# Kernel tuning notes

Measured on AMD Instinct MI355X. Metric: run time of the kernel, lower is better.

## Reference

```python
import jax, jax.numpy as jnp
import numpy as np
from jax import lax

T, B, F, H, C = 1024, 128, 88, 1024, 88


def setup_inputs() -> dict:
    key = jax.random.key(0)
    ks = jax.random.split(key, 8)
    s = 0.02
    lengths = jnp.sort(jax.random.randint(ks[1], (B,), 1, T + 1))[::-1]  # descending, as pack_padded requires
    return {
        "input_sequences": jax.random.normal(ks[0], (T, B, F), dtype=jnp.float32),
        "input_sequence_lengths": lengths.astype(jnp.int64),
        "W_ih": jax.random.normal(ks[2], (4 * H, F), dtype=jnp.float32) * s,
        "W_hh": jax.random.normal(ks[3], (4 * H, H), dtype=jnp.float32) * s,
        "b_ih": jax.random.normal(ks[4], (4 * H,), dtype=jnp.float32) * s,
        "b_hh": jax.random.normal(ks[5], (4 * H,), dtype=jnp.float32) * s,
        "W_fc": jax.random.normal(ks[6], (C, H), dtype=jnp.float32) * s,
        "b_fc": jax.random.normal(ks[7], (C,), dtype=jnp.float32) * s,
    }


def reference(input_sequences, input_sequence_lengths, W_ih, W_hh, b_ih, b_hh, W_fc, b_fc):
    Tn, Bn, _ = input_sequences.shape
    Hn = W_hh.shape[1]
    # mask[t, b] = True iff timestep t is within sequence b (equivalent to :batch_size_t slicing
    # when lengths are sorted descending, as the torch code assumes)
    mask_seq = jnp.arange(Tn)[:, None] < input_sequence_lengths[None, :]  # [T, B]

    h0 = jnp.zeros((Bn, Hn), dtype=input_sequences.dtype)
    c0 = jnp.zeros((Bn, Hn), dtype=input_sequences.dtype)

    def step(carry, inp):
        h, c = carry
        x, m = inp  # x: [B, F], m: [B]
        gates = x @ W_ih.T + b_ih + h @ W_hh.T + b_hh  # [B, 4H], order i,f,g,o
        i, f, g, o = jnp.split(gates, 4, axis=1)
        c_new = jax.nn.sigmoid(f) * c + jax.nn.sigmoid(i) * jnp.tanh(g)
        h_new = jax.nn.sigmoid(o) * jnp.tanh(c_new)
        mb = m[:, None]
        h2 = jnp.where(mb, h_new, h)
        c2 = jnp.where(mb, c_new, c)
        logits_t = jnp.where(mb, h2 @ W_fc.T + b_fc, 0.0)  # rows beyond batch_size_t stay zero
        return (h2, c2), logits_t

    (_, _), predictions = lax.scan(step, (h0, c0), (input_sequences, mask_seq))  # [T, B, C]

    logits = jnp.transpose(predictions, (1, 0, 2))  # [B, T, C]
    binary_logits = jnp.stack((logits, 1.0 - logits), axis=3)  # [B, T, C, 2]
    return binary_logits.reshape(-1, 2)
```

## Files before the change

### kernel.cpp

```cpp
#include <hip/hip_runtime.h>
#include <cstdint>
#include <cstddef>

#define T_STEPS 1024
#define B_SZ    128
#define F_SZ    88
#define H_SZ    1024
#define C_SZ    88

#define N_GATE_WG 128
#define N_FC_WG   6
#define N_COMPUTE (N_GATE_WG + N_FC_WG)
#define N_WG      N_COMPUTE
#define BLOCK     128
#define FLAG_STRIDE 16
#define RING      16

typedef __attribute__((ext_vector_type(8)))  __bf16 bf16x8;
typedef __attribute__((ext_vector_type(16))) float  f32x16;
typedef __attribute__((ext_vector_type(4)))  int    i32x4;

#define SLAB_OFF    0
#define SLAB_BYTES  (64 * 1024 * 2)
#define BIAS_OFF    (SLAB_OFF + SLAB_BYTES)
#define LENL_OFF    (BIAS_OFF + 256)
#define NB_OFF      (LENL_OFF + 512)
#define EXCH_OFF    (NB_OFF + 2064)
#define EXCH_WAVE   (32 * 68 * 4)
#define STAGE_OFF   (EXCH_OFF + 2 * EXCH_WAVE)
#define SMEM_BYTES  (STAGE_OFF + 2 * 512 * 2)

#define HBUF_ELEMS  131072
#define HBUF_BYTES  (HBUF_ELEMS * 2)

__device__ __forceinline__ float sigm(float x) {
    return __builtin_amdgcn_rcpf(1.0f + __expf(-x));
}
__device__ __forceinline__ float tanh_fast(float x) {
    return 1.0f - 2.0f * __builtin_amdgcn_rcpf(__expf(2.0f * x) + 1.0f);
}
__device__ __forceinline__ void st_llc(void* p, uint64_t v) {
    __hip_atomic_store((uint64_t*)p, v, __ATOMIC_RELAXED,
                       __HIP_MEMORY_SCOPE_AGENT);
}

extern "C" __global__ void __launch_bounds__(BLOCK, 1)
lstm_fused(const float* __restrict__ X,
           const int*   __restrict__ len_raw,
           const float* __restrict__ W_ih,
           const float* __restrict__ W_hh,
           const float* __restrict__ b_ih,
           const float* __restrict__ b_hh,
           const float* __restrict__ W_fc,
           const float* __restrict__ b_fc,
           float*       __restrict__ out,
           __bf16*      __restrict__ hbuf,
           int*         __restrict__ flags)
{
    extern __shared__ char smem[];
    __bf16*         slab  = (__bf16*)(smem + SLAB_OFF);
    float*          biasL = (float*)(smem + BIAS_OFF);
    int*            lenL  = (int*)(smem + LENL_OFF);
    unsigned short* nbL   = (unsigned short*)(smem + NB_OFF);

    const int  wg   = blockIdx.x;
    const int  tid  = threadIdx.x;
    const int  w    = tid >> 6;
    const int  lane = tid & 63;
    const int  col  = lane & 31;
    const int  h5   = lane >> 5;
    const bool isGate = (wg < N_GATE_WG);

    int ug = 0, bt2 = 0, cg = 0;
    if (isGate) { int m = wg >> 3, x = wg & 7; bt2 = x >> 2; ug = 4 * m + (x & 3); }
    else        { int f = wg - N_GATE_WG; bt2 = f / 3; cg = f % 3; }
    const int bti  = bt2 * 2 + w;
    const int fidx = bt2 * 68 + (isGate ? ug : (64 + cg));
    const int hbase = bt2 * 68;

    const int lstride = (len_raw[1] == 0) ? 2 : 1;
    if (tid < B_SZ) lenL[tid] = len_raw[tid * lstride];
    __syncthreads();
    for (int t = tid; t <= T_STEPS; t += BLOCK) {
        int cnt = 0;
        #pragma unroll 4
        for (int b = 0; b < B_SZ; ++b) cnt += (lenL[b] > t) ? 1 : 0;
        nbL[t] = (unsigned short)cnt;
    }

    bf16x8 wih[2][6];
    if (isGate) {
        for (int idx = tid; idx < 64 * 1024; idx += BLOCK) {
            int cc2 = idx >> 10, k = idx & 1023;
            int n = cc2 >> 5, cc = cc2 & 31;
            int gate = cc & 3, ul = cc >> 2;
            int j = ug * 16 + n * 8 + ul;
            float v = W_hh[(size_t)(gate * H_SZ + j) * H_SZ + k];
            slab[(size_t)((k >> 4) * 128 + n * 64 + ((k >> 3) & 1) * 32 + cc) * 8 + (k & 7)] = (__bf16)v;
        }
        {
            const int gate = col & 3, ul = col >> 2;
            #pragma unroll
            for (int n = 0; n < 2; ++n) {
                const float* wrow = W_ih + (size_t)(gate * H_SZ + ug * 16 + n * 8 + ul) * F_SZ;
                #pragma unroll
                for (int kt = 0; kt < 6; ++kt) {
                    const int f0 = kt * 16 + h5 * 8;
                    bf16x8 b;
                    #pragma unroll
                    for (int e = 0; e < 8; ++e) {
                        int k = f0 + e;
                        b[e] = (k < F_SZ) ? (__bf16)wrow[k] : (__bf16)0.0f;
                    }
                    wih[n][kt] = b;
                }
            }
        }
        if (tid < 64) {
            int n = tid >> 5, cc = tid & 31, gate = cc & 3, ul = cc >> 2;
            int row = gate * H_SZ + ug * 16 + n * 8 + ul;
            biasL[tid] = b_ih[row] + b_hh[row];
        }
    } else {
        for (int idx = tid; idx < 32 * 1024; idx += BLOCK) {
            int cc = idx >> 10, k = idx & 1023;
            int c = cg * 32 + cc;
            float v = (c < C_SZ) ? W_fc[(size_t)c * H_SZ + k] : 0.0f;
            slab[(size_t)((k >> 4) * 64 + ((k >> 3) & 1) * 32 + cc) * 8 + (k & 7)] = (__bf16)v;
        }
        if (tid < 32) {
            int c = cg * 32 + tid;
            biasL[tid] = (c < C_SZ) ? b_fc[c] : 0.0f;
        }
    }

    __syncthreads();
    if (tid == 0) {
        __builtin_amdgcn_s_waitcnt(0);
        __hip_atomic_store(flags + fidx * FLAG_STRIDE, 1, __ATOMIC_RELAXED,
                           __HIP_MEMORY_SCOPE_AGENT);
    }

    const int a4    = col & 3;
    const int u0    = col >> 2;
    const int c0fc  = cg * 32;
    const int phase = wg & (RING - 1);

    float*  exch   = (float*)(smem + EXCH_OFF) + w * (EXCH_WAVE / 4);
    __bf16* stageW = (__bf16*)(smem + STAGE_OFF) + w * 512;

    const bool hasFC = (lane < 3);
    long guard = 0;

    float c_reg[8] = {0.f,0.f,0.f,0.f,0.f,0.f,0.f,0.f};
    float h_reg[8] = {0.f,0.f,0.f,0.f,0.f,0.f,0.f,0.f};

    for (int t = 0; t <= T_STEPS; ++t) {
        const int nb_t   = (t < T_STEPS) ? (int)nbL[t] : 0;
        const int nb_pre = (t > 0) ? (int)nbL[t - 1] : B_SZ;
        const __bf16* hin  = hbuf + (size_t)((t + RING - 1) & (RING - 1)) * HBUF_ELEMS;
        __bf16*       hout = hbuf + (size_t)(t & (RING - 1)) * HBUF_ELEMS;

        const bool gcomp = isGate && (t < T_STEPS) && (bti * 32 < nb_t);
        const bool gwrt  = isGate && (t < T_STEPS) && (bti * 32 < nb_pre);

        f32x16 acc[2];

        if (gcomp) {
            #pragma unroll
            for (int n = 0; n < 2; ++n) {
                float bv = biasL[n * 32 + col];
                #pragma unroll
                for (int i = 0; i < 16; ++i) acc[n][i] = bv;
            }
            const float* xrow = X + ((size_t)t * B_SZ + (bti * 32 + col)) * F_SZ;
            #pragma unroll
            for (int kt = 0; kt < 6; ++kt) {
                int f0 = kt * 16 + h5 * 8;
                bf16x8 a;
                if (f0 < F_SZ) {
                    float4 lo = *(const float4*)(xrow + f0);
                    float4 hi = *(const float4*)(xrow + f0 + 4);
                    a[0] = (__bf16)lo.x; a[1] = (__bf16)lo.y; a[2] = (__bf16)lo.z; a[3] = (__bf16)lo.w;
                    a[4] = (__bf16)hi.x; a[5] = (__bf16)hi.y; a[6] = (__bf16)hi.z; a[7] = (__bf16)hi.w;
                } else {
                    #pragma unroll
                    for (int j = 0; j < 8; ++j) a[j] = (__bf16)0.0f;
                }
                #pragma unroll
                for (int n = 0; n < 2; ++n)
                    acc[n] = __builtin_amdgcn_mfma_f32_32x32x16_bf16(a, wih[n][kt], acc[n], 0, 0, 0);
            }
        }

        if (w == 0) {
            const int target = t + 1;
            for (;;) {
                int a = __hip_atomic_load(flags + (hbase + lane) * FLAG_STRIDE,
                                          __ATOMIC_RELAXED, __HIP_MEMORY_SCOPE_AGENT);
                int b = hasFC ? __hip_atomic_load(flags + (hbase + 64 + lane) * FLAG_STRIDE,
                                                  __ATOMIC_RELAXED, __HIP_MEMORY_SCOPE_AGENT)
                              : target;
                if (__all((a >= target) && (b >= target))) break;
                __builtin_amdgcn_s_sleep(1);
                if (++guard > 400000000L) break;
            }
        }
        __syncthreads();

        if (((t + phase) & (RING - 1)) == 0) {
            if (tid == 0)
                __builtin_amdgcn_fence(__ATOMIC_ACQUIRE, "agent");
            __syncthreads();
        }

        if (!isGate && tid == 0) {
            __hip_atomic_store(flags + fidx * FLAG_STRIDE, t + 2, __ATOMIC_RELAXED,
                               __HIP_MEMORY_SCOPE_AGENT);
        }

        if (!isGate && t >= 1) {
            const int  s        = t - 1;
            const int  nb_s     = (int)nbL[s];
            const bool act_tile = (bti * 32) < nb_s;
            f32x16 accf;
            #pragma unroll
            for (int i = 0; i < 16; ++i) accf[i] = 0.0f;
            if (act_tile) {
                float bv = biasL[col];
                #pragma unroll
                for (int i = 0; i < 16; ++i) accf[i] = bv;
                const __bf16* hA = hin + (size_t)bti * 512 + (size_t)lane * 8;
                const __bf16* bB = slab + lane * 8;
                #pragma unroll 8
                for (int kt = 0; kt < 64; ++kt) {
                    bf16x8 a = __builtin_bit_cast(bf16x8, *(const i32x4*)(hA + (size_t)kt * 2048));
                    bf16x8 b = __builtin_bit_cast(bf16x8, *(const i32x4*)(bB + (size_t)kt * 512));
                    accf = __builtin_amdgcn_mfma_f32_32x32x16_bf16(a, b, accf, 0, 0, 0);
                }
            }
            const int c = c0fc + col;
            if (c < C_SZ) {
                #pragma unroll
                for (int i = 0; i < 16; ++i) {
                    int row = (i & 3) + 8 * (i >> 2) + 4 * h5;
                    int b   = bti * 32 + row;
                    float v = (act_tile && b < nb_s) ? accf[i] : 0.0f;
                    float2 o2; o2.x = v; o2.y = 1.0f - v;
                    *(float2*)(out + ((size_t)(b * T_STEPS + s) * C_SZ + c) * 2) = o2;
                }
            }
        }

        if (gcomp && t > 0) {
            const __bf16* hA = hin + (size_t)bti * 512 + (size_t)lane * 8;
            const __bf16* bB = slab + lane * 8;
            i32x4 pf0[16], pf1[16];
            #pragma unroll
            for (int i = 0; i < 16; ++i)
                pf0[i] = *(const i32x4*)(hA + (size_t)i * 2048);
            __builtin_amdgcn_sched_barrier(0);
            #pragma unroll
            for (int c = 0; c < 4; ++c) {
                i32x4 (&cur)[16] = (c & 1) ? pf1 : pf0;
                i32x4 (&nxt)[16] = (c & 1) ? pf0 : pf1;
                if (c < 3) {
                    #pragma unroll
                    for (int i = 0; i < 16; ++i)
                        nxt[i] = *(const i32x4*)(hA + (size_t)((c + 1) * 16 + i) * 2048);
                }
                __builtin_amdgcn_sched_barrier(0);
                #pragma unroll
                for (int i = 0; i < 16; ++i) {
                    bf16x8 a = __builtin_bit_cast(bf16x8, cur[i]);
                    const int ks = c * 16 + i;
                    bf16x8 b0 = __builtin_bit_cast(bf16x8,
                        *(const i32x4*)(bB + (size_t)ks * 1024));
                    acc[0] = __builtin_amdgcn_mfma_f32_32x32x16_bf16(a, b0, acc[0], 0, 0, 0);
                    bf16x8 b1 = __builtin_bit_cast(bf16x8,
                        *(const i32x4*)(bB + (size_t)ks * 1024 + 512));
                    acc[1] = __builtin_amdgcn_mfma_f32_32x32x16_bf16(a, b1, acc[1], 0, 0, 0);
                }
                __builtin_amdgcn_sched_barrier(0);
            }
        }
        if (gcomp) {
            #pragma unroll
            for (int n = 0; n < 2; ++n)
                #pragma unroll
                for (int j = 0; j < 16; ++j)
                    exch[(n * 16 + j) * 68 + lane] = acc[n][j];
        }
        __syncthreads();

        if (gcomp) {
            #pragma unroll
            for (int n = 0; n < 2; ++n) {
                #pragma unroll
                for (int q = 0; q < 4; ++q) {
                    const float4 v = *(const float4*)(exch + (n * 16 + 4 * a4 + q) * 68 + 32 * h5 + (col & ~3));
                    float si = sigm(v.x);
                    float sf = sigm(v.y);
                    float tg = tanh_fast(v.z);
                    float so = sigm(v.w);
                    float cn = sf * c_reg[n * 4 + q] + si * tg;
                    float hn = so * tanh_fast(cn);
                    int b = bti * 32 + 8 * a4 + 4 * h5 + q;
                    if (b < nb_t) { c_reg[n * 4 + q] = cn; h_reg[n * 4 + q] = hn; }
                }
            }
        }
        if (gwrt) {
            #pragma unroll
            for (int n = 0; n < 2; ++n)
                #pragma unroll
                for (int q = 0; q < 4; ++q)
                    stageW[(8 * a4 + 4 * h5 + q) * 16 + n * 8 + u0] = (__bf16)h_reg[n * 4 + q];
        }
        __syncthreads();

        if (gwrt) {
            const uint64_t* sp = (const uint64_t*)(stageW + (size_t)col * 16 + (size_t)h5 * 8);
            uint64_t* hp = (uint64_t*)(hout + (size_t)ug * 2048 + (size_t)bti * 512 + (size_t)lane * 8);
            st_llc(hp,     sp[0]);
            st_llc(hp + 1, sp[1]);
        }
        __syncthreads();

        if (isGate && tid == 0) {
            __builtin_amdgcn_s_waitcnt(0);
            __hip_atomic_store(flags + fidx * FLAG_STRIDE, t + 2, __ATOMIC_RELAXED,
                               __HIP_MEMORY_SCOPE_AGENT);
        }
    }
}

extern "C" void kernel_launch(void* const* d_in, const int* in_sizes, int n_in,
                              void* d_out, int out_size, void* d_ws, size_t ws_size,
                              hipStream_t stream) {
    const float* X    = (const float*)d_in[0];
    const int*   lens = (const int*)d_in[1];
    const float* Wih  = (const float*)d_in[2];
    const float* Whh  = (const float*)d_in[3];
    const float* bih  = (const float*)d_in[4];
    const float* bhh  = (const float*)d_in[5];
    const float* Wfc  = (const float*)d_in[6];
    const float* bfc  = (const float*)d_in[7];
    float*       outp = (float*)d_out;

    __bf16* hbuf  = (__bf16*)d_ws;
    int*    flags = (int*)((char*)d_ws + (size_t)RING * HBUF_BYTES);

    (void)hipFuncSetAttribute((const void*)lstm_fused,
                              hipFuncAttributeMaxDynamicSharedMemorySize, SMEM_BYTES);

    void* args[] = { (void*)&X, (void*)&lens, (void*)&Wih, (void*)&Whh,
                     (void*)&bih, (void*)&bhh, (void*)&Wfc, (void*)&bfc,
                     (void*)&outp, (void*)&hbuf, (void*)&flags };
    hipError_t le = hipLaunchCooperativeKernel((void*)lstm_fused, dim3(N_WG), dim3(BLOCK),
                                               args, (unsigned)SMEM_BYTES, stream);
    if (le != hipSuccess) {
        hipLaunchKernelGGL(lstm_fused, dim3(N_WG), dim3(BLOCK),
                           (unsigned)SMEM_BYTES, stream,
                           X, lens, Wih, Whh, bih, bhh, Wfc, bfc, outp, hbuf, flags);
    }
}
```

Baseline: 7.885 ms.

## Split gate recurrent GEMM K dimension across two waves per tile

```diff
diff --git a/kernel.cpp b/kernel.cpp
--- a/kernel.cpp
+++ b/kernel.cpp
@@ -12,7 +12,7 @@
 #define N_FC_WG   6
 #define N_COMPUTE (N_GATE_WG + N_FC_WG)
 #define N_WG      N_COMPUTE
-#define BLOCK     128
+#define BLOCK     256
 #define FLAG_STRIDE 16
 #define RING      16
 
@@ -26,8 +26,8 @@
 #define LENL_OFF    (BIAS_OFF + 256)
 #define NB_OFF      (LENL_OFF + 512)
 #define EXCH_OFF    (NB_OFF + 2064)
-#define EXCH_WAVE   (32 * 68 * 4)
-#define STAGE_OFF   (EXCH_OFF + 2 * EXCH_WAVE)
+#define EXCH_TILE   (32 * 68 * 4)
+#define STAGE_OFF   (EXCH_OFF + 2 * EXCH_TILE)
 #define SMEM_BYTES  (STAGE_OFF + 2 * 512 * 2)
 
 #define HBUF_ELEMS  131072
@@ -71,11 +71,14 @@
     const int  h5   = lane >> 5;
     const bool isGate = (wg < N_GATE_WG);
 
+    const int  tile = w >> 1;
+    const int  kh   = w & 1;
+
     int ug = 0, bt2 = 0, cg = 0;
     if (isGate) { int m = wg >> 3, x = wg & 7; bt2 = x >> 2; ug = 4 * m + (x & 3); }
     else        { int f = wg - N_GATE_WG; bt2 = f / 3; cg = f % 3; }
-    const int bti  = bt2 * 2 + w;
-    const int fidx = bt2 * 68 + (isGate ? ug : (64 + cg));
+    const int bti  = bt2 * 2 + (isGate ? tile : w);
+    const int fidx  = bt2 * 68 + (isGate ? ug : (64 + cg));
     const int hbase = bt2 * 68;
 
     const int lstride = (len_raw[1] == 0) ? 2 : 1;
@@ -87,8 +90,10 @@
         for (int b = 0; b < B_SZ; ++b) cnt += (lenL[b] > t) ? 1 : 0;
         nbL[t] = (unsigned short)cnt;
     }
-
-    bf16x8 wih[2][6];
+    for (int idx = tid; idx < 2 * (EXCH_TILE / 4); idx += BLOCK)
+        ((float*)(smem + EXCH_OFF))[idx] = 0.0f;
+
+    bf16x8 wih[2][3];
     if (isGate) {
         for (int idx = tid; idx < 64 * 1024; idx += BLOCK) {
             int cc2 = idx >> 10, k = idx & 1023;
@@ -104,15 +109,15 @@
             for (int n = 0; n < 2; ++n) {
                 const float* wrow = W_ih + (size_t)(gate * H_SZ + ug * 16 + n * 8 + ul) * F_SZ;
                 #pragma unroll
-                for (int kt = 0; kt < 6; ++kt) {
-                    const int f0 = kt * 16 + h5 * 8;
+                for (int j = 0; j < 3; ++j) {
+                    const int f0 = (kh * 3 + j) * 16 + h5 * 8;
                     bf16x8 b;
                     #pragma unroll
                     for (int e = 0; e < 8; ++e) {
                         int k = f0 + e;
                         b[e] = (k < F_SZ) ? (__bf16)wrow[k] : (__bf16)0.0f;
                     }
-                    wih[n][kt] = b;
+                    wih[n][j] = b;
                 }
             }
         }
@@ -146,8 +151,8 @@
     const int c0fc  = cg * 32;
     const int phase = wg & (RING - 1);
 
-    float*  exch   = (float*)(smem + EXCH_OFF) + w * (EXCH_WAVE / 4);
-    __bf16* stageW = (__bf16*)(smem + STAGE_OFF) + w * 512;
+    float*  exchT  = (float*)(smem + EXCH_OFF) + tile * (EXCH_TILE / 4);
+    __bf16* stageW = (__bf16*)(smem + STAGE_OFF) + tile * 512;
 
     const bool hasFC = (lane < 3);
     long guard = 0;
@@ -169,14 +174,14 @@
         if (gcomp) {
             #pragma unroll
             for (int n = 0; n < 2; ++n) {
-                float bv = biasL[n * 32 + col];
+                float bv = (kh == 0) ? biasL[n * 32 + col] : 0.0f;
                 #pragma unroll
                 for (int i = 0; i < 16; ++i) acc[n][i] = bv;
             }
             const float* xrow = X + ((size_t)t * B_SZ + (bti * 32 + col)) * F_SZ;
             #pragma unroll
-            for (int kt = 0; kt < 6; ++kt) {
-                int f0 = kt * 16 + h5 * 8;
+            for (int j = 0; j < 3; ++j) {
+                int f0 = (kh * 3 + j) * 16 + h5 * 8;
                 bf16x8 a;
                 if (f0 < F_SZ) {
                     float4 lo = *(const float4*)(xrow + f0);
@@ -185,11 +190,11 @@
                     a[4] = (__bf16)hi.x; a[5] = (__bf16)hi.y; a[6] = (__bf16)hi.z; a[7] = (__bf16)hi.w;
                 } else {
                     #pragma unroll
-                    for (int j = 0; j < 8; ++j) a[j] = (__bf16)0.0f;
+                    for (int e = 0; e < 8; ++e) a[e] = (__bf16)0.0f;
                 }
                 #pragma unroll
                 for (int n = 0; n < 2; ++n)
-                    acc[n] = __builtin_amdgcn_mfma_f32_32x32x16_bf16(a, wih[n][kt], acc[n], 0, 0, 0);
+                    acc[n] = __builtin_amdgcn_mfma_f32_32x32x16_bf16(a, wih[n][j], acc[n], 0, 0, 0);
             }
         }
 
@@ -219,7 +224,7 @@
                                __HIP_MEMORY_SCOPE_AGENT);
         }
 
-        if (!isGate && t >= 1) {
+        if (!isGate && w < 2 && t >= 1) {
             const int  s        = t - 1;
             const int  nb_s     = (int)nbL[s];
             const bool act_tile = (bti * 32) < nb_s;
@@ -253,52 +258,45 @@
         }
 
         if (gcomp && t > 0) {
-            const __bf16* hA = hin + (size_t)bti * 512 + (size_t)lane * 8;
+            const __bf16* hA = hin + (size_t)(kh * 32) * 2048
+                                   + (size_t)bti * 512 + (size_t)lane * 8;
             const __bf16* bB = slab + lane * 8;
-            i32x4 pf0[16], pf1[16];
-            #pragma unroll
-            for (int i = 0; i < 16; ++i)
-                pf0[i] = *(const i32x4*)(hA + (size_t)i * 2048);
+            i32x4 pf[32];
+            #pragma unroll
+            for (int i = 0; i < 32; ++i)
+                pf[i] = *(const i32x4*)(hA + (size_t)i * 2048);
             __builtin_amdgcn_sched_barrier(0);
             #pragma unroll
-            for (int c = 0; c < 4; ++c) {
-                i32x4 (&cur)[16] = (c & 1) ? pf1 : pf0;
-                i32x4 (&nxt)[16] = (c & 1) ? pf0 : pf1;
-                if (c < 3) {
-                    #pragma unroll
-                    for (int i = 0; i < 16; ++i)
-                        nxt[i] = *(const i32x4*)(hA + (size_t)((c + 1) * 16 + i) * 2048);
-                }
-                __builtin_amdgcn_sched_barrier(0);
-                #pragma unroll
-                for (int i = 0; i < 16; ++i) {
-                    bf16x8 a = __builtin_bit_cast(bf16x8, cur[i]);
-                    const int ks = c * 16 + i;
-                    bf16x8 b0 = __builtin_bit_cast(bf16x8,
-                        *(const i32x4*)(bB + (size_t)ks * 1024));
-                    acc[0] = __builtin_amdgcn_mfma_f32_32x32x16_bf16(a, b0, acc[0], 0, 0, 0);
-                    bf16x8 b1 = __builtin_bit_cast(bf16x8,
-                        *(const i32x4*)(bB + (size_t)ks * 1024 + 512));
-                    acc[1] = __builtin_amdgcn_mfma_f32_32x32x16_bf16(a, b1, acc[1], 0, 0, 0);
-                }
-                __builtin_amdgcn_sched_barrier(0);
-            }
+            for (int i = 0; i < 32; ++i) {
+                bf16x8 a = __builtin_bit_cast(bf16x8, pf[i]);
+                const int ks = kh * 32 + i;
+                bf16x8 b0 = __builtin_bit_cast(bf16x8,
+                    *(const i32x4*)(bB + (size_t)ks * 1024));
+                acc[0] = __builtin_amdgcn_mfma_f32_32x32x16_bf16(a, b0, acc[0], 0, 0, 0);
+                bf16x8 b1 = __builtin_bit_cast(bf16x8,
+                    *(const i32x4*)(bB + (size_t)ks * 1024 + 512));
+                acc[1] = __builtin_amdgcn_mfma_f32_32x32x16_bf16(a, b1, acc[1], 0, 0, 0);
+            }
+            __builtin_amdgcn_sched_barrier(0);
         }
         if (gcomp) {
             #pragma unroll
             for (int n = 0; n < 2; ++n)
                 #pragma unroll
                 for (int j = 0; j < 16; ++j)
-                    exch[(n * 16 + j) * 68 + lane] = acc[n][j];
+                    atomicAdd(&exchT[(n * 16 + j) * 68 + lane], acc[n][j]);
         }
         __syncthreads();
 
-        if (gcomp) {
+        if (gcomp && kh == 0) {
             #pragma unroll
             for (int n = 0; n < 2; ++n) {
                 #pragma unroll
                 for (int q = 0; q < 4; ++q) {
-                    const float4 v = *(const float4*)(exch + (n * 16 + 4 * a4 + q) * 68 + 32 * h5 + (col & ~3));
+                    float4* vp = (float4*)(exchT + (n * 16 + 4 * a4 + q) * 68 + 32 * h5 + (col & ~3));
+                    const float4 v = *vp;
+                    float4 z; z.x = 0.f; z.y = 0.f; z.z = 0.f; z.w = 0.f;
+                    *vp = z;
                     float si = sigm(v.x);
                     float sf = sigm(v.y);
                     float tg = tanh_fast(v.z);
@@ -310,7 +308,7 @@
                 }
             }
         }
-        if (gwrt) {
+        if (gwrt && kh == 0) {
             #pragma unroll
             for (int n = 0; n < 2; ++n)
                 #pragma unroll
@@ -319,7 +317,7 @@
         }
         __syncthreads();
 
-        if (gwrt) {
+        if (gwrt && kh == 0) {
             const uint64_t* sp = (const uint64_t*)(stageW + (size_t)col * 16 + (size_t)h5 * 8);
             uint64_t* hp = (uint64_t*)(hout + (size_t)ug * 2048 + (size_t)bti * 512 + (size_t)lane * 8);
             st_llc(hp,     sp[0]);
```

Result: slower. 15.09 ms (+91.4%).
